# Performance work log

Hardware: AMD Instinct MI355X
Metric: run time of the kernel (lower is better)

The kernel has to match this reference:

```python
import jax, jax.numpy as jnp
import numpy as np

D_MODEL = 1024
NHEAD = 16
D_HEAD = D_MODEL // NHEAD


def setup_inputs() -> dict:
    key = jax.random.key(0)
    ks = jax.random.split(key, 9)
    s = 1.0 / np.sqrt(D_MODEL)
    x = jax.random.normal(ks[0], (4, 2048, D_MODEL), dtype=jnp.float32)
    Wq = jax.random.uniform(ks[1], (D_MODEL, D_MODEL), jnp.float32, -s, s)
    bq = jax.random.uniform(ks[2], (D_MODEL,), jnp.float32, -s, s)
    Wk = jax.random.uniform(ks[3], (D_MODEL, D_MODEL), jnp.float32, -s, s)
    bk = jax.random.uniform(ks[4], (D_MODEL,), jnp.float32, -s, s)
    Wv = jax.random.uniform(ks[5], (D_MODEL, D_MODEL), jnp.float32, -s, s)
    bv = jax.random.uniform(ks[6], (D_MODEL,), jnp.float32, -s, s)
    Wo = jax.random.uniform(ks[7], (D_MODEL, D_MODEL), jnp.float32, -s, s)
    bo = jax.random.uniform(ks[8], (D_MODEL,), jnp.float32, -s, s)
    return {"x": x, "Wq": Wq, "bq": bq, "Wk": Wk, "bk": bk,
            "Wv": Wv, "bv": bv, "Wo": Wo, "bo": bo}


def reference(x, Wq, bq, Wk, bk, Wv, bv, Wo, bo):
    B, T, _ = x.shape
    # project and split heads: [B, H, T, Dh]
    def heads(y):
        return y.reshape(B, T, NHEAD, D_HEAD).transpose(0, 2, 1, 3)
    Q = heads(x @ Wq + bq)
    K = heads(x @ Wk + bk)
    V = heads(x @ Wv + bv)
    scores = jnp.einsum('bhqd,bhkd->bhqk', Q, K) / jnp.sqrt(
        jnp.asarray(D_HEAD, x.dtype))
    attn = jax.nn.softmax(scores, axis=-1)  # dropout: eval mode (identity)
    out = jnp.einsum('bhqk,bhkd->bhqd', attn, V)
    out = out.transpose(0, 2, 1, 3).reshape(B, T, D_MODEL)
    return out @ Wo + bo
```

## Files before the change

### kernel.cpp

```cpp
#include <hip/hip_runtime.h>
#include <hip/hip_bf16.h>

typedef unsigned short u16;
typedef u16  u16x8 __attribute__((ext_vector_type(8)));
typedef u16  u16x4 __attribute__((ext_vector_type(4)));
typedef short bf16x8 __attribute__((ext_vector_type(8)));
typedef float f32x4 __attribute__((ext_vector_type(4)));

#define D_MODEL 1024
#define T_SEQ   2048
#define BATCH   4
#define NHEAD   16
#define DHEAD   64
#define MROWS   (BATCH*T_SEQ)
#define K2LOG2E 0.18033688011112042f

#define MFMA(a,b,c) __builtin_amdgcn_mfma_f32_16x16x32_bf16(a,b,c,0,0,0)

__device__ __forceinline__ u16 f2bf(float f) {
  __hip_bfloat16 h = __float2bfloat16(f);
  u16 r; __builtin_memcpy(&r, &h, 2); return r;
}
__device__ __forceinline__ unsigned cvtpk(float lo, float hi) {
  unsigned r;
  asm("v_cvt_pk_bf16_f32 %0, %1, %2" : "=v"(r) : "v"(lo), "v"(hi));
  return r;
}

__device__ __forceinline__ void gload16(const void* g, void* l) {
  __builtin_amdgcn_global_load_lds(
      (const __attribute__((address_space(1))) void*)g,
      (__attribute__((address_space(3))) void*)l, 16, 0, 0);
}

__device__ __forceinline__ int xcd_swz(int f, int cpx) {
  return (f & 7) * cpx + (f >> 3);
}

__global__ void cvt_x_kernel(const float* __restrict__ x, u16* __restrict__ xb, int n8) {
  int i = blockIdx.x * blockDim.x + threadIdx.x;
  if (i >= n8) return;
  const f32x4* p = (const f32x4*)(x + (size_t)i * 8);
  f32x4 a = p[0], b = p[1];
  union { u16x8 v; unsigned u[4]; } o;
  o.u[0] = cvtpk(a[0], a[1]); o.u[1] = cvtpk(a[2], a[3]);
  o.u[2] = cvtpk(b[0], b[1]); o.u[3] = cvtpk(b[2], b[3]);
  *(u16x8*)(xb + (size_t)i * 8) = o.v;
}

__global__ void transpose_w_kernel(const float* __restrict__ w0, const float* __restrict__ w1,
                                   const float* __restrict__ w2, const float* __restrict__ w3,
                                   u16* __restrict__ o0, u16* __restrict__ o1,
                                   u16* __restrict__ o2, u16* __restrict__ o3) {
  const float* W; u16* O;
  if      (blockIdx.z == 0) { W = w0; O = o0; }
  else if (blockIdx.z == 1) { W = w1; O = o1; }
  else if (blockIdx.z == 2) { W = w2; O = o2; }
  else                      { W = w3; O = o3; }
  __shared__ float t[32][33];
  int tx = threadIdx.x, ty = threadIdx.y;
  int k0 = blockIdx.y * 32, n0 = blockIdx.x * 32;
#pragma unroll
  for (int j = 0; j < 4; j++)
    t[ty + 8 * j][tx] = W[(size_t)(k0 + ty + 8 * j) * D_MODEL + n0 + tx];
  __syncthreads();
#pragma unroll
  for (int j = 0; j < 4; j++)
    O[(size_t)(n0 + ty + 8 * j) * D_MODEL + k0 + tx] = f2bf(t[tx][ty + 8 * j]);
}

template<int BF16OUT>
__device__ __forceinline__ void gemm_body(const u16* __restrict__ A, const u16* __restrict__ Bt,
                                          const float* __restrict__ bias, void* __restrict__ outp,
                                          int M, int N, int K, float oscale, int trans,
                                          int m0, int n0) {
  __shared__ u16 As[2][128 * 64];
  __shared__ u16 Bs[2][128 * 64];
  int tid = threadIdx.x;
  int lane = tid & 63, w = tid >> 6;
  int l15 = lane & 15, hi = lane >> 4;
  int wr = w >> 1, wc = w & 1;
  int srow = lane >> 3, su = lane & 7;
  f32x4 acc[4][4] = {};

  const u16* ap[4]; const u16* bp[4];
#pragma unroll
  for (int p = 0; p < 4; p++) {
    int row = (w * 4 + p) * 8 + srow;
    int cb  = su ^ (row & 7);
    ap[p] = A  + (size_t)(m0 + row) * K + cb * 8;
    bp[p] = Bt + (size_t)(n0 + row) * K + cb * 8;
  }

#pragma unroll
  for (int p = 0; p < 4; p++) {
    gload16(ap[p], &As[0][(w * 4 + p) * 512]);
    gload16(bp[p], &Bs[0][(w * 4 + p) * 512]);
    ap[p] += 64; bp[p] += 64;
  }
  __syncthreads();

  const int NK = K / 64;
  for (int kk = 0; kk < NK; kk++) {
    int cur = kk & 1;
    if (kk + 1 < NK) {
      int nxt = cur ^ 1;
#pragma unroll
      for (int p = 0; p < 4; p++) {
        gload16(ap[p], &As[nxt][(w * 4 + p) * 512]);
        gload16(bp[p], &Bs[nxt][(w * 4 + p) * 512]);
        ap[p] += 64; bp[p] += 64;
      }
    }
#pragma unroll
    for (int s = 0; s < 2; s++) {
      bf16x8 af[4], bfr[4];
#pragma unroll
      for (int i = 0; i < 4; i++) {
        int ra = wr * 64 + i * 16 + l15;
        af[i]  = *(const bf16x8*)&As[cur][ra * 64 + ((s * 4 + hi) ^ (ra & 7)) * 8];
        int rb = wc * 64 + i * 16 + l15;
        bfr[i] = *(const bf16x8*)&Bs[cur][rb * 64 + ((s * 4 + hi) ^ (rb & 7)) * 8];
      }
      __builtin_amdgcn_s_setprio(1);
#pragma unroll
      for (int i = 0; i < 4; i++)
#pragma unroll
        for (int j = 0; j < 4; j++)
          acc[i][j] = MFMA(af[i], bfr[j], acc[i][j]);
      __builtin_amdgcn_s_setprio(0);
    }
    __syncthreads();
  }

  if (trans) {
#pragma unroll
    for (int j = 0; j < 4; j++) {
      int n = n0 + wc * 64 + j * 16 + l15;
      float bv = bias[n];
#pragma unroll
      for (int i = 0; i < 4; i++) {
        int mb = m0 + wr * 64 + i * 16 + hi * 4;
        int off = mb & 63;
        int colp = (off & 32) + (((off >> 2) & 3) << 3) + (((off >> 4) & 1) << 2);
        union { u16x4 v; unsigned u[2]; } t;
        t.u[0] = cvtpk((acc[i][j][0] + bv) * oscale, (acc[i][j][1] + bv) * oscale);
        t.u[1] = cvtpk((acc[i][j][2] + bv) * oscale, (acc[i][j][3] + bv) * oscale);
        *(u16x4*)((u16*)outp + (size_t)n * M + (mb - off) + colp) = t.v;
      }
    }
  } else {
#pragma unroll
    for (int j = 0; j < 4; j++) {
      int n = n0 + wc * 64 + j * 16 + l15;
      float bv = bias[n];
#pragma unroll
      for (int i = 0; i < 4; i++) {
        int mbase = m0 + wr * 64 + i * 16 + hi * 4;
#pragma unroll
        for (int r = 0; r < 4; r++) {
          float v = (acc[i][j][r] + bv) * oscale;
          if (BF16OUT) ((u16*)outp)[(size_t)(mbase + r) * N + n] = f2bf(v);
          else        ((float*)outp)[(size_t)(mbase + r) * N + n] = v;
        }
      }
    }
  }
}

__global__ __launch_bounds__(256) void gemm_qkv_kernel(
    const u16* __restrict__ A,
    const u16* __restrict__ Btq, const u16* __restrict__ Btk, const u16* __restrict__ Btv,
    const float* __restrict__ bq, const float* __restrict__ bk, const float* __restrict__ bv,
    u16* __restrict__ oq, u16* __restrict__ ok, u16* __restrict__ ov) {
  int f = (blockIdx.z * 64 + blockIdx.y) * 8 + blockIdx.x;
  int wk = xcd_swz(f, 192);
  int bx = wk & 7, by = (wk >> 3) & 63, bz = wk >> 9;
  const u16* Bt; const float* bias; u16* o; float sc; int tr;
  if      (bz == 0) { Bt = Btq; bias = bq; o = oq; sc = K2LOG2E; tr = 0; }
  else if (bz == 1) { Bt = Btk; bias = bk; o = ok; sc = 1.0f; tr = 0; }
  else              { Bt = Btv; bias = bv; o = ov; sc = 1.0f; tr = 1; }
  gemm_body<1>(A, Bt, bias, o, MROWS, D_MODEL, D_MODEL, sc, tr, by * 128, bx * 128);
}

__global__ __launch_bounds__(256) void gemm_f32out_kernel(
    const u16* __restrict__ A, const u16* __restrict__ Bt,
    const float* __restrict__ bias, float* __restrict__ out) {
  int f = blockIdx.y * 8 + blockIdx.x;
  int wk = xcd_swz(f, 64);
  int bx = wk & 7, by = wk >> 3;
  gemm_body<0>(A, Bt, bias, out, MROWS, D_MODEL, D_MODEL, 1.0f, 0, by * 128, bx * 128);
}

__global__ __launch_bounds__(512) void attn_kernel(
    const u16* __restrict__ Qb, const u16* __restrict__ Kb,
    const u16* __restrict__ Vt, u16* __restrict__ Ob) {
  __shared__ u16 Ks[2][64 * 64];
  __shared__ u16 Vs[2][64 * 64];
  int tid = threadIdx.x;
  int lane = tid & 63, w = tid >> 6;
  int l15 = lane & 15, hi = lane >> 4;
  int f = (blockIdx.z * NHEAD + blockIdx.y) * (T_SEQ / 128) + blockIdx.x;
  int wwg = xcd_swz(f, 128);
  int bx = wwg & 15, h = (wwg >> 4) & 15, b = wwg >> 8;
  int q0 = bx * 128 + w * 16;
  size_t headoff = (size_t)b * T_SEQ * D_MODEL + h * DHEAD;
  const u16* vhead = Vt + (size_t)h * DHEAD * MROWS + (size_t)b * T_SEQ;

  const u16* qp = Qb + headoff + (size_t)(q0 + l15) * D_MODEL;
  bf16x8 qf0 = *(const bf16x8*)(qp + hi * 8);
  bf16x8 qf1 = *(const bf16x8*)(qp + 32 + hi * 8);

  f32x4 o[4] = {};
  f32x4 lsum = {};
  bf16x8 vones;
  { union { bf16x8 v; u16 e[8]; } c;
#pragma unroll
    for (int j = 0; j < 8; j++) c.e[j] = 0x3F80;
    vones = c.v; }

  int r0 = tid >> 3, cu = tid & 7;
  int cb = cu ^ (r0 & 7);
  const u16* ksrc = Kb + headoff + (size_t)r0 * D_MODEL + cb * 8;
  const u16* vsrc = vhead + (size_t)r0 * MROWS + cb * 8;

  gload16(ksrc, &Ks[0][w * 512]);
  gload16(vsrc, &Vs[0][w * 512]);
  ksrc += 64 * D_MODEL; vsrc += 64;
  __syncthreads();

  const int NT = T_SEQ / 64;
  for (int kt = 0; kt < NT; kt++) {
    int cur = kt & 1;
    if (kt + 1 < NT) {
      int nxt = cur ^ 1;
      gload16(ksrc, &Ks[nxt][w * 512]);
      gload16(vsrc, &Vs[nxt][w * 512]);
      ksrc += 64 * D_MODEL; vsrc += 64;
    }

    f32x4 s[4];
    __builtin_amdgcn_s_setprio(1);
#pragma unroll
    for (int sub = 0; sub < 4; sub++) {
      int ra = sub * 16 + l15;
      bf16x8 kf0 = *(const bf16x8*)&Ks[cur][ra * 64 + ((0 + hi) ^ (ra & 7)) * 8];
      bf16x8 kf1 = *(const bf16x8*)&Ks[cur][ra * 64 + ((4 + hi) ^ (ra & 7)) * 8];
      f32x4 z = {};
      z = MFMA(kf0, qf0, z); z = MFMA(kf1, qf1, z);
      s[sub] = z;
    }
    __builtin_amdgcn_s_setprio(0);

    bf16x8 vf[4][2];
#pragma unroll
    for (int dt = 0; dt < 4; dt++) {
      int rv = dt * 16 + l15;
#pragma unroll
      for (int ks = 0; ks < 2; ks++)
        vf[dt][ks] = *(const bf16x8*)&Vs[cur][rv * 64 + ((ks * 4 + hi) ^ (rv & 7)) * 8];
    }

#pragma unroll
    for (int sub = 0; sub < 4; sub++)
#pragma unroll
      for (int r = 0; r < 4; r++)
        s[sub][r] = __builtin_amdgcn_exp2f(s[sub][r]);

    union PB { bf16x8 v; unsigned u[4]; };
    PB pb[2];
#pragma unroll
    for (int ks = 0; ks < 2; ks++) {
      pb[ks].u[0] = cvtpk(s[2*ks][0],   s[2*ks][1]);
      pb[ks].u[1] = cvtpk(s[2*ks][2],   s[2*ks][3]);
      pb[ks].u[2] = cvtpk(s[2*ks+1][0], s[2*ks+1][1]);
      pb[ks].u[3] = cvtpk(s[2*ks+1][2], s[2*ks+1][3]);
    }

    __builtin_amdgcn_s_setprio(1);
#pragma unroll
    for (int ks = 0; ks < 2; ks++) {
#pragma unroll
      for (int dt = 0; dt < 4; dt++)
        o[dt] = MFMA(vf[dt][ks], pb[ks].v, o[dt]);
      lsum = MFMA(vones, pb[ks].v, lsum);
    }
    __builtin_amdgcn_s_setprio(0);

    __syncthreads();
  }

  float rs = 1.0f / lsum[0];
  u16* op = Ob + headoff + (size_t)(q0 + l15) * D_MODEL + hi * 4;
#pragma unroll
  for (int dt = 0; dt < 4; dt++) {
    union { u16x4 v; unsigned u[2]; } wo;
    wo.u[0] = cvtpk(o[dt][0] * rs, o[dt][1] * rs);
    wo.u[1] = cvtpk(o[dt][2] * rs, o[dt][3] * rs);
    *(u16x4*)(op + dt * 16) = wo.v;
  }
}

extern "C" void kernel_launch(void* const* d_in, const int* in_sizes, int n_in,
                              void* d_out, int out_size, void* d_ws, size_t ws_size,
                              hipStream_t stream) {
  const float* x  = (const float*)d_in[0];
  const float* Wq = (const float*)d_in[1];
  const float* bq = (const float*)d_in[2];
  const float* Wk = (const float*)d_in[3];
  const float* bk = (const float*)d_in[4];
  const float* Wv = (const float*)d_in[5];
  const float* bv = (const float*)d_in[6];
  const float* Wo = (const float*)d_in[7];
  const float* bo = (const float*)d_in[8];

  char* ws = (char*)d_ws;
  u16* xb  = (u16*)(ws);
  u16* wqt = (u16*)(ws + ((size_t)16 << 20));
  u16* wkt = (u16*)(ws + ((size_t)18 << 20));
  u16* wvt = (u16*)(ws + ((size_t)20 << 20));
  u16* wot = (u16*)(ws + ((size_t)22 << 20));
  u16* qb  = (u16*)(ws + ((size_t)24 << 20));
  u16* kb  = (u16*)(ws + ((size_t)40 << 20));
  u16* vtb = (u16*)(ws + ((size_t)56 << 20));
  u16* ab  = (u16*)(ws + ((size_t)72 << 20));

  cvt_x_kernel<<<(MROWS * D_MODEL / 8 + 255) / 256, 256, 0, stream>>>(x, xb, MROWS * D_MODEL / 8);
  transpose_w_kernel<<<dim3(32, 32, 4), dim3(32, 8), 0, stream>>>(Wq, Wk, Wv, Wo, wqt, wkt, wvt, wot);
  gemm_qkv_kernel<<<dim3(D_MODEL / 128, MROWS / 128, 3), 256, 0, stream>>>(
      xb, wqt, wkt, wvt, bq, bk, bv, qb, kb, vtb);
  attn_kernel<<<dim3(T_SEQ / 128, NHEAD, BATCH), 512, 0, stream>>>(qb, kb, vtb, ab);
  gemm_f32out_kernel<<<dim3(D_MODEL / 128, MROWS / 128), 256, 0, stream>>>(ab, wot, bo, (float*)d_out);
}
```

Before: 174.3 us.

## Triple-buffer attention K/V loads with vmcnt waits; vectorize weight transpose

The attention kernel goes from double to triple buffering of its K/V shared-memory tiles. It prefetches two tiles ahead and replaces the full __syncthreads with an explicit s_waitcnt vmcnt(2) plus s_barrier, so one tile's global loads can stay in flight across the barrier. The weight transpose kernel now uses 64x64 tiles with float4 loads and packed 16-byte bf16 stores instead of scalar accesses. The cost is extra LDS per block, which may lower occupancy, and hand-counted vmcnt waits that depend on how many loads gload16 issues.

Result: no change. 174.8 us (+0.3%).

```diff
diff --git a/kernel.cpp b/kernel.cpp
--- a/kernel.cpp
+++ b/kernel.cpp
@@ -57,16 +57,27 @@
   else if (blockIdx.z == 1) { W = w1; O = o1; }
   else if (blockIdx.z == 2) { W = w2; O = o2; }
   else                      { W = w3; O = o3; }
-  __shared__ float t[32][33];
-  int tx = threadIdx.x, ty = threadIdx.y;
-  int k0 = blockIdx.y * 32, n0 = blockIdx.x * 32;
-#pragma unroll
-  for (int j = 0; j < 4; j++)
-    t[ty + 8 * j][tx] = W[(size_t)(k0 + ty + 8 * j) * D_MODEL + n0 + tx];
+  __shared__ float t[64][65];
+  int tid = threadIdx.x;
+  int k0 = blockIdx.y * 64, n0 = blockIdx.x * 64;
+  int lr = tid >> 4, lc = (tid & 15) * 4;
+#pragma unroll
+  for (int j = 0; j < 4; j++) {
+    int row = j * 16 + lr;
+    f32x4 v = *(const f32x4*)(W + (size_t)(k0 + row) * D_MODEL + n0 + lc);
+    t[row][lc] = v[0]; t[row][lc + 1] = v[1]; t[row][lc + 2] = v[2]; t[row][lc + 3] = v[3];
+  }
   __syncthreads();
-#pragma unroll
-  for (int j = 0; j < 4; j++)
-    O[(size_t)(n0 + ty + 8 * j) * D_MODEL + k0 + tx] = f2bf(t[tx][ty + 8 * j]);
+  int nr = tid >> 2, ks = (tid & 3) * 16;
+  union { u16x8 v; unsigned u[4]; } a, b;
+#pragma unroll
+  for (int i = 0; i < 4; i++) {
+    a.u[i] = cvtpk(t[ks + 2 * i][nr],     t[ks + 2 * i + 1][nr]);
+    b.u[i] = cvtpk(t[ks + 8 + 2 * i][nr], t[ks + 9 + 2 * i][nr]);
+  }
+  u16* op = O + (size_t)(n0 + nr) * D_MODEL + k0 + ks;
+  *(u16x8*)op = a.v;
+  *(u16x8*)(op + 8) = b.v;
 }
 
 template<int BF16OUT>
@@ -195,8 +206,8 @@
 __global__ __launch_bounds__(512) void attn_kernel(
     const u16* __restrict__ Qb, const u16* __restrict__ Kb,
     const u16* __restrict__ Vt, u16* __restrict__ Ob) {
-  __shared__ u16 Ks[2][64 * 64];
-  __shared__ u16 Vs[2][64 * 64];
+  __shared__ u16 Ks[3][64 * 64];
+  __shared__ u16 Vs[3][64 * 64];
   int tid = threadIdx.x;
   int lane = tid & 63, w = tid >> 6;
   int l15 = lane & 15, hi = lane >> 4;
@@ -227,25 +238,31 @@
   gload16(ksrc, &Ks[0][w * 512]);
   gload16(vsrc, &Vs[0][w * 512]);
   ksrc += 64 * D_MODEL; vsrc += 64;
-  __syncthreads();
+  gload16(ksrc, &Ks[1][w * 512]);
+  gload16(vsrc, &Vs[1][w * 512]);
+  ksrc += 64 * D_MODEL; vsrc += 64;
+  asm volatile("s_waitcnt vmcnt(2)" ::: "memory");
+  __builtin_amdgcn_s_barrier();
+  __builtin_amdgcn_sched_barrier(0);
 
   const int NT = T_SEQ / 64;
-  for (int kt = 0; kt < NT; kt++) {
-    int cur = kt & 1;
-    if (kt + 1 < NT) {
-      int nxt = cur ^ 1;
-      gload16(ksrc, &Ks[nxt][w * 512]);
-      gload16(vsrc, &Vs[nxt][w * 512]);
+  int bufc = 0, bufs = 2;
+  for (int t = 0; t < NT; t++) {
+    if (t + 2 < NT) {
+      gload16(ksrc, &Ks[bufs][w * 512]);
+      gload16(vsrc, &Vs[bufs][w * 512]);
       ksrc += 64 * D_MODEL; vsrc += 64;
     }
+    const u16* kb_ = &Ks[bufc][0];
+    const u16* vb_ = &Vs[bufc][0];
 
     f32x4 s[4];
     __builtin_amdgcn_s_setprio(1);
 #pragma unroll
     for (int sub = 0; sub < 4; sub++) {
       int ra = sub * 16 + l15;
-      bf16x8 kf0 = *(const bf16x8*)&Ks[cur][ra * 64 + ((0 + hi) ^ (ra & 7)) * 8];
-      bf16x8 kf1 = *(const bf16x8*)&Ks[cur][ra * 64 + ((4 + hi) ^ (ra & 7)) * 8];
+      bf16x8 kf0 = *(const bf16x8*)&kb_[ra * 64 + ((0 + hi) ^ (ra & 7)) * 8];
+      bf16x8 kf1 = *(const bf16x8*)&kb_[ra * 64 + ((4 + hi) ^ (ra & 7)) * 8];
       f32x4 z = {};
       z = MFMA(kf0, qf0, z); z = MFMA(kf1, qf1, z);
       s[sub] = z;
@@ -258,7 +275,7 @@
       int rv = dt * 16 + l15;
 #pragma unroll
       for (int ks = 0; ks < 2; ks++)
-        vf[dt][ks] = *(const bf16x8*)&Vs[cur][rv * 64 + ((ks * 4 + hi) ^ (rv & 7)) * 8];
+        vf[dt][ks] = *(const bf16x8*)&vb_[rv * 64 + ((ks * 4 + hi) ^ (rv & 7)) * 8];
     }
 
 #pragma unroll
@@ -287,7 +304,16 @@
     }
     __builtin_amdgcn_s_setprio(0);
 
-    __syncthreads();
+    if (t + 2 < NT) {
+      asm volatile("s_waitcnt vmcnt(2)" ::: "memory");
+    } else {
+      asm volatile("s_waitcnt vmcnt(0)" ::: "memory");
+    }
+    __builtin_amdgcn_s_barrier();
+    __builtin_amdgcn_sched_barrier(0);
+
+    bufc = (bufc == 2) ? 0 : bufc + 1;
+    bufs = (bufs == 2) ? 0 : bufs + 1;
   }
 
   float rs = 1.0f / lsum[0];
@@ -326,7 +352,7 @@
   u16* ab  = (u16*)(ws + ((size_t)72 << 20));
 
   cvt_x_kernel<<<(MROWS * D_MODEL / 8 + 255) / 256, 256, 0, stream>>>(x, xb, MROWS * D_MODEL / 8);
-  transpose_w_kernel<<<dim3(32, 32, 4), dim3(32, 8), 0, stream>>>(Wq, Wk, Wv, Wo, wqt, wkt, wvt, wot);
+  transpose_w_kernel<<<dim3(16, 16, 4), 256, 0, stream>>>(Wq, Wk, Wv, Wo, wqt, wkt, wvt, wot);
   gemm_qkv_kernel<<<dim3(D_MODEL / 128, MROWS / 128, 3), 256, 0, stream>>>(
       xb, wqt, wkt, wvt, bq, bk, bv, qb, kb, vtb);
   attn_kernel<<<dim3(T_SEQ / 128, NHEAD, BATCH), 512, 0, stream>>>(qb, kb, vtb, ab);
```
